# Optimization experiments

Measured on AMD Instinct MI355X. Metric: run time of the kernel, lower is better.

Reference implementation:

```python
import jax, jax.numpy as jnp
import numpy as np

SIZE = 20
STRIDE = 5
EPS = 1e-8


def setup_inputs() -> dict:
    key = jax.random.key(0)
    x = jax.random.normal(key, (256, 32, 2048), dtype=jnp.float32)
    return {"x": x}


def reference(x):
    B, F, L = x.shape
    T = (L - SIZE) // STRIDE + 1
    # gather sliding windows: [B, F, T, SIZE]
    starts = jnp.arange(T) * STRIDE
    idx = starts[:, None] + jnp.arange(SIZE)  # [T, SIZE]
    w = x[:, :, idx]
    # center each window along the window axis
    c = w - w.mean(axis=-1, keepdims=True)           # [B, F, T, S]
    n = jnp.sqrt(jnp.sum(c * c, axis=-1))            # [B, F, T]
    # pairwise cross products of centered windows across all feature pairs
    cross = jnp.einsum('bits,bjts->bijt', c, c)      # [B, F, F, T]
    i, j = jnp.triu_indices(F, k=1)                  # row-major upper triangle == torch loop order
    num = cross[:, i, j, :]                          # [B, P, T]
    den = n[:, i, :] * n[:, j, :] + EPS              # [B, P, T]
    return num / den
```

## Files before the change

kernel.cpp:

```cpp
#include <hip/hip_runtime.h>

typedef _Float16 half2_t __attribute__((ext_vector_type(2)));
typedef _Float16 f16x8   __attribute__((ext_vector_type(8)));
typedef float    f32x16  __attribute__((ext_vector_type(16)));

#define TPB    256
#define NF     32
#define T_TOT  406
#define LLEN   2048
#define NPAIR  496
#define NCH    29
#define WPB    14
#define W2S    36
#define ZS     32
#define OTS    8

__device__ __forceinline__ float dot2(unsigned int a, unsigned int b, float c) {
    return __builtin_amdgcn_fdot2(__builtin_bit_cast(half2_t, a),
                                  __builtin_bit_cast(half2_t, b), c, false);
}
__device__ __forceinline__ unsigned int pkrtz(float a, float b) {
    return __builtin_bit_cast(unsigned int, __builtin_amdgcn_cvt_pkrtz(a, b));
}

__global__ __launch_bounds__(TPB)
void tscorr_kernel(const float* __restrict__ x, float* __restrict__ out) {
    __shared__ union {
        unsigned int W2[2][44][W2S];
        unsigned int ot[NPAIR * OTS];
    } R;
    __shared__ unsigned int Zs[WPB * 10 * ZS];

    const int tid = threadIdx.x;

    const int n     = blockIdx.x;
    const int xcd   = n & 7;
    const int slot  = n >> 3;
    const int bidx  = slot / NCH;
    const int chunk = slot - bidx * NCH;
    const int b     = xcd + 8 * bidx;

    const int l0     = chunk * (WPB * 5);
    const int lstart = l0 & ~3;
    const int off    = l0 - lstart;
    const float* xb  = x + (size_t)b * NF * LLEN;

    {
        const int f  = tid >> 3;
        const int p4 = tid & 7;
        #pragma unroll
        for (int it = 0; it < 3; ++it) {
            const int grp = p4 + it * 8;
            if (grp < 22) {
                const int pos = grp * 4;
                const float4 v = *(const float4*)&xb[f * LLEN + lstart + pos];
                const float v4 = (lstart + pos + 4 < LLEN)
                                     ? xb[f * LLEN + lstart + pos + 4] : 0.f;
                R.W2[0][2 * grp    ][f] = pkrtz(v.x, v.y);
                R.W2[0][2 * grp + 1][f] = pkrtz(v.z, v.w);
                R.W2[1][2 * grp    ][f] = pkrtz(v.y, v.z);
                R.W2[1][2 * grp + 1][f] = pkrtz(v.w, v4);
            }
        }
    }
    __syncthreads();

    {
        const unsigned int ONES = 0x3C003C00u;
        for (int idx = tid; idx < NF * WPB; idx += TPB) {
            const int t   = idx >> 5;
            const int ff  = idx & 31;
            const int par = t & 1;
            const int ms  = (off + 5 * t - par) >> 1;
            const unsigned int* p0 = &R.W2[par][ms][ff];
            unsigned int h[10];
            float S = 0.f, G = 0.f;
            #pragma unroll
            for (int q = 0; q < 10; ++q) {
                h[q] = p0[q * W2S];
                S = dot2(h[q], ONES, S);
                G = dot2(h[q], h[q], G);
            }
            const float nn = sqrtf(fmaxf(G - S * S * 0.05f, 0.f));
            const float rn = __builtin_amdgcn_rcpf(fmaxf(nn, 1e-6f));
            const float mb = -(S * 0.05f) * rn;
            unsigned int* zo = &Zs[(t * 10) * ZS + ff];
            #pragma unroll
            for (int q = 0; q < 10; ++q) {
                const half2_t hp = __builtin_bit_cast(half2_t, h[q]);
                const float z0 = fmaf((float)hp.x, rn, mb);
                const float z1 = fmaf((float)hp.y, rn, mb);
                zo[q * ZS] = pkrtz(z0, z1);
            }
        }
    }
    __syncthreads();

    {
        const int wv   = tid >> 6;
        const int lane = tid & 63;
        const int j    = lane & 31;
        const int hi   = lane >> 5;

        for (int pr = wv; pr < 7; pr += 4) {
            f32x16 C0, C1;
            #pragma unroll
            for (int r = 0; r < 16; ++r) { C0[r] = 0.f; C1[r] = 0.f; }

            #pragma unroll
            for (int w = 0; w < 2; ++w) {
                const int t = 2 * pr + w;
                const unsigned int* base = &Zs[(t * 10 + 4 * hi) * ZS + j];
                union { unsigned int u[4]; f16x8 h; } u1;
                u1.u[0] = base[0];
                u1.u[1] = base[ZS];
                u1.u[2] = base[2 * ZS];
                u1.u[3] = base[3 * ZS];
                union { unsigned int u[4]; f16x8 h; } u2;
                u2.u[2] = 0u; u2.u[3] = 0u;
                if (hi == 0) {
                    const unsigned int* b2 = &Zs[(t * 10 + 8) * ZS + j];
                    u2.u[0] = b2[0];
                    u2.u[1] = b2[ZS];
                } else { u2.u[0] = 0u; u2.u[1] = 0u; }
                if (w == 0) {
                    C0 = __builtin_amdgcn_mfma_f32_32x32x16_f16(u1.h, u1.h, C0, 0, 0, 0);
                    C0 = __builtin_amdgcn_mfma_f32_32x32x16_f16(u2.h, u2.h, C0, 0, 0, 0);
                } else {
                    C1 = __builtin_amdgcn_mfma_f32_32x32x16_f16(u1.h, u1.h, C1, 0, 0, 0);
                    C1 = __builtin_amdgcn_mfma_f32_32x32x16_f16(u2.h, u2.h, C1, 0, 0, 0);
                }
            }

            #pragma unroll
            for (int r = 0; r < 16; ++r) {
                const int il = (r & 3) + 8 * (r >> 2);
                const int i  = il + 4 * hi;
                if (j > i) {
                    const int p = i * (63 - i) / 2 + (j - i - 1);
                    R.ot[p * OTS + ((pr + p) & 7)] = pkrtz(C0[r], C1[r]);
                }
            }
        }
    }
    __syncthreads();

    float* ob = out + (size_t)b * NPAIR * T_TOT + chunk * WPB;
    for (int k = tid; k < NPAIR * OTS; k += TPB) {
        const int p   = k >> 3;
        const int slt = k & 7;
        const int wpo = (slt - p) & 7;
        if (wpo < 7) {
            const half2_t h = __builtin_bit_cast(half2_t, R.ot[k]);
            float2 o;
            o.x = (float)h.x;
            o.y = (float)h.y;
            *(float2*)&ob[(size_t)p * T_TOT + 2 * wpo] = o;
        }
    }
}

extern "C" void kernel_launch(void* const* d_in, const int* in_sizes, int n_in,
                              void* d_out, int out_size, void* d_ws, size_t ws_size,
                              hipStream_t stream) {
    (void)in_sizes; (void)n_in; (void)out_size; (void)d_ws; (void)ws_size;
    const float* x = (const float*)d_in[0];
    float* out     = (float*)d_out;
    const int nblocks = 8 * 32 * NCH;
    hipLaunchKernelGGL(tscorr_kernel, dim3(nblocks), dim3(TPB), 0, stream, x, out);
}
```

Measured before the change: 62.84 us.

## Double block size to 512 threads and vectorize shared-memory output readback

Raises the block to 512 threads so each of the 7 MFMA wave tasks and each normalization item gets its own wave or thread, removing the strided loops. The transposed output staging now uses an XOR swizzle of the wave index, so each thread reads 4 consecutive slots with a uint4 and writes up to 4 float2 values. The MFMA-to-LDS store loop precomputes the triangle index base per lane. Costs: one of the 8 waves sits idle in the MFMA phase, larger blocks may lower occupancy, and it relies on swizzle bank-conflict behaviour.

```diff
diff --git a/kernel.cpp b/kernel.cpp
--- a/kernel.cpp
+++ b/kernel.cpp
@@ -4,7 +4,7 @@
 typedef _Float16 f16x8   __attribute__((ext_vector_type(8)));
 typedef float    f32x16  __attribute__((ext_vector_type(16)));
 
-#define TPB    256
+#define TPB    512
 #define NF     32
 #define T_TOT  406
 #define LLEN   2048
@@ -46,11 +46,11 @@
     const float* xb  = x + (size_t)b * NF * LLEN;
 
     {
-        const int f  = tid >> 3;
-        const int p4 = tid & 7;
+        const int f  = tid >> 4;
+        const int g0 = tid & 15;
         #pragma unroll
-        for (int it = 0; it < 3; ++it) {
-            const int grp = p4 + it * 8;
+        for (int it = 0; it < 2; ++it) {
+            const int grp = g0 + it * 16;
             if (grp < 22) {
                 const int pos = grp * 4;
                 const float4 v = *(const float4*)&xb[f * LLEN + lstart + pos];
@@ -65,33 +65,31 @@
     }
     __syncthreads();
 
-    {
+    if (tid < NF * WPB) {
         const unsigned int ONES = 0x3C003C00u;
-        for (int idx = tid; idx < NF * WPB; idx += TPB) {
-            const int t   = idx >> 5;
-            const int ff  = idx & 31;
-            const int par = t & 1;
-            const int ms  = (off + 5 * t - par) >> 1;
-            const unsigned int* p0 = &R.W2[par][ms][ff];
-            unsigned int h[10];
-            float S = 0.f, G = 0.f;
-            #pragma unroll
-            for (int q = 0; q < 10; ++q) {
-                h[q] = p0[q * W2S];
-                S = dot2(h[q], ONES, S);
-                G = dot2(h[q], h[q], G);
-            }
-            const float nn = sqrtf(fmaxf(G - S * S * 0.05f, 0.f));
-            const float rn = __builtin_amdgcn_rcpf(fmaxf(nn, 1e-6f));
-            const float mb = -(S * 0.05f) * rn;
-            unsigned int* zo = &Zs[(t * 10) * ZS + ff];
-            #pragma unroll
-            for (int q = 0; q < 10; ++q) {
-                const half2_t hp = __builtin_bit_cast(half2_t, h[q]);
-                const float z0 = fmaf((float)hp.x, rn, mb);
-                const float z1 = fmaf((float)hp.y, rn, mb);
-                zo[q * ZS] = pkrtz(z0, z1);
-            }
+        const int t   = tid >> 5;
+        const int ff  = tid & 31;
+        const int par = t & 1;
+        const int ms  = (off + 5 * t - par) >> 1;
+        const unsigned int* p0 = &R.W2[par][ms][ff];
+        unsigned int h[10];
+        float S = 0.f, G = 0.f;
+        #pragma unroll
+        for (int q = 0; q < 10; ++q) {
+            h[q] = p0[q * W2S];
+            S = dot2(h[q], ONES, S);
+            G = dot2(h[q], h[q], G);
+        }
+        const float nn = sqrtf(fmaxf(G - S * S * 0.05f, 0.f));
+        const float rn = __builtin_amdgcn_rcpf(fmaxf(nn, 1e-6f));
+        const float mb = -(S * 0.05f) * rn;
+        unsigned int* zo = &Zs[(t * 10) * ZS + ff];
+        #pragma unroll
+        for (int q = 0; q < 10; ++q) {
+            const half2_t hp = __builtin_bit_cast(half2_t, h[q]);
+            const float z0 = fmaf((float)hp.x, rn, mb);
+            const float z1 = fmaf((float)hp.y, rn, mb);
+            zo[q * ZS] = pkrtz(z0, z1);
         }
     }
     __syncthreads();
@@ -99,10 +97,11 @@
     {
         const int wv   = tid >> 6;
         const int lane = tid & 63;
-        const int j    = lane & 31;
+        const int jz   = lane & 31;
         const int hi   = lane >> 5;
 
-        for (int pr = wv; pr < 7; pr += 4) {
+        if (wv < 7) {
+            const int pr = wv;
             f32x16 C0, C1;
             #pragma unroll
             for (int r = 0; r < 16; ++r) { C0[r] = 0.f; C1[r] = 0.f; }
@@ -110,7 +109,7 @@
             #pragma unroll
             for (int w = 0; w < 2; ++w) {
                 const int t = 2 * pr + w;
-                const unsigned int* base = &Zs[(t * 10 + 4 * hi) * ZS + j];
+                const unsigned int* base = &Zs[(t * 10 + 4 * hi) * ZS + jz];
                 union { unsigned int u[4]; f16x8 h; } u1;
                 u1.u[0] = base[0];
                 u1.u[1] = base[ZS];
@@ -119,7 +118,7 @@
                 union { unsigned int u[4]; f16x8 h; } u2;
                 u2.u[2] = 0u; u2.u[3] = 0u;
                 if (hi == 0) {
-                    const unsigned int* b2 = &Zs[(t * 10 + 8) * ZS + j];
+                    const unsigned int* b2 = &Zs[(t * 10 + 8) * ZS + jz];
                     u2.u[0] = b2[0];
                     u2.u[1] = b2[ZS];
                 } else { u2.u[0] = 0u; u2.u[1] = 0u; }
@@ -132,13 +131,16 @@
                 }
             }
 
+            const int i   = jz;
+            const int tri = i * (63 - i) / 2;
+            const int pbh = tri - i - 1 + 4 * hi;
+            const int thr = i - 4 * hi;
             #pragma unroll
             for (int r = 0; r < 16; ++r) {
-                const int il = (r & 3) + 8 * (r >> 2);
-                const int i  = il + 4 * hi;
-                if (j > i) {
-                    const int p = i * (63 - i) / 2 + (j - i - 1);
-                    R.ot[p * OTS + ((pr + p) & 7)] = pkrtz(C0[r], C1[r]);
+                const int jl = (r & 3) + 8 * (r >> 2);
+                if (jl > thr) {
+                    const int p = pbh + jl;
+                    R.ot[p * OTS + (pr ^ (p & 4))] = pkrtz(C0[r], C1[r]);
                 }
             }
         }
@@ -146,16 +148,23 @@
     __syncthreads();
 
     float* ob = out + (size_t)b * NPAIR * T_TOT + chunk * WPB;
-    for (int k = tid; k < NPAIR * OTS; k += TPB) {
-        const int p   = k >> 3;
-        const int slt = k & 7;
-        const int wpo = (slt - p) & 7;
-        if (wpo < 7) {
-            const half2_t h = __builtin_bit_cast(half2_t, R.ot[k]);
-            float2 o;
-            o.x = (float)h.x;
-            o.y = (float)h.y;
-            *(float2*)&ob[(size_t)p * T_TOT + 2 * wpo] = o;
+    for (int k = tid; k < NPAIR * 2; k += TPB) {
+        const int p  = k >> 1;
+        const int h  = k & 1;
+        const int p4 = (p >> 2) & 1;
+        const int hp = h ^ p4;
+        const uint4 v = *(const uint4*)&R.ot[p * OTS + h * 4];
+        float* po = &ob[(size_t)p * T_TOT + 8 * hp];
+        const unsigned int u[4] = {v.x, v.y, v.z, v.w};
+        #pragma unroll
+        for (int e = 0; e < 4; ++e) {
+            if (hp == 0 || e < 3) {
+                const half2_t hh = __builtin_bit_cast(half2_t, u[e]);
+                float2 o;
+                o.x = (float)hh.x;
+                o.y = (float)hh.y;
+                *(float2*)&po[2 * e] = o;
+            }
         }
     }
 }
```

Result: slower. 95.92 us (+52.6%).
